# Kernel tuning notes

Measured on AMD Instinct MI355X. Metric: run time of the kernel, lower is better.

The kernel has to match this reference:

```python
import jax, jax.numpy as jnp
import numpy as np

# --- SLAYER params (nmnistNet.yaml) ---
THETA = 10.0
TS = 1.0
TAU_REF = 1.0
SCALE_REF = 2.0
T_SAMPLE = 300
B = 8

def _alpha_kernel(tau, mult, t_sample, ts, eps=0.01):
    vals = []
    t = 0.0
    while t < t_sample:
        v = mult * t / tau * np.exp(1.0 - t / tau)
        if abs(v) < eps and t > tau:
            break
        vals.append(v)
        t += ts
    return np.asarray(vals, np.float32)

# refractory kernel: alpha kernel with mult = -scaleRef*theta (slayer._calculateRefKernel)
REF_KERNEL = _alpha_kernel(TAU_REF, -SCALE_REF * THETA, T_SAMPLE, TS)
NREF = REF_KERNEL.shape[0]  # 11 for these params; REF_KERNEL[0] == 0


def spike(u):
    """slayerCuda.getSpikes: per-neuron sequential threshold recurrence over time.
    u: [..., T] membrane potential. On spike at t, REF_KERNEL is accumulated
    into u[t:t+NREF]; spike amplitude is 1/Ts."""
    uT = jnp.moveaxis(u, -1, 0)  # [T, ...]
    refk = jnp.asarray(REF_KERNEL[1:]).reshape((NREF - 1,) + (1,) * (u.ndim - 1))
    buf0 = jnp.zeros((NREF - 1,) + uT.shape[1:], u.dtype)  # pending refractory

    def step(buf, u_t):
        u_mod = u_t + buf[0]
        ev = (u_mod >= THETA).astype(u.dtype)
        buf = jnp.concatenate([buf[1:], jnp.zeros_like(buf[:1])], axis=0) + ev[None] * refk
        return buf, ev / TS

    _, s = jax.lax.scan(step, buf0, uT)
    return jnp.moveaxis(s, 0, -1)


def conv2d_t(x, w, pad):
    """slayer.conv: Conv3d with kernel (k,k,1) == per-timestep 2D conv.
    x: [B,C,H,W,T], w: [O,I,kh,kw]."""
    b, c, h, wd, t = x.shape
    xb = jnp.moveaxis(x, -1, 1).reshape(b * t, c, h, wd)
    y = jax.lax.conv_general_dilated(xb, w, (1, 1), [(pad, pad), (pad, pad)],
                                     dimension_numbers=('NCHW', 'OIHW', 'NCHW'))
    o, ho, wo = y.shape[1], y.shape[2], y.shape[3]
    return jnp.moveaxis(y.reshape(b, t, o, ho, wo), 1, -1)


def sum_pool2(x):
    """slayer.pool(2): fixed-weight (1.1*theta) 2x2/stride-2 sum over H,W per channel."""
    y = jax.lax.reduce_window(x, 0.0, jax.lax.add, (1, 1, 2, 2, 1), (1, 1, 2, 2, 1), 'VALID')
    return 1.1 * THETA * y


def setup_inputs():
    key = jax.random.key(0)
    k0, k1, k2, k3, k4 = jax.random.split(key, 5)
    spikeInput = (jax.random.uniform(k0, (B, 2, 34, 34, T_SAMPLE)) < 0.1).astype(jnp.float32) / TS
    # conv weights: kaiming-uniform bound * 100 (the __init__ scales conv weights by 100)
    w1 = jax.random.uniform(k1, (16, 2, 5, 5), minval=-14.1, maxval=14.1, dtype=jnp.float32)
    w2 = jax.random.uniform(k2, (32, 16, 3, 3), minval=-8.3, maxval=8.3, dtype=jnp.float32)
    w3 = jax.random.uniform(k3, (64, 32, 3, 3), minval=-5.9, maxval=5.9, dtype=jnp.float32)
    wfc = jax.random.uniform(k4, (10, 64, 8, 8), minval=-0.5, maxval=0.5, dtype=jnp.float32)
    return {"spikeInput": spikeInput, "w1": w1, "w2": w2, "w3": w3, "wfc": wfc}


def reference(spikeInput, w1, w2, w3, wfc):
    s1 = spike(conv2d_t(spikeInput, w1, 1))  # [B,16,32,32,T]
    s2 = spike(sum_pool2(s1))                # [B,16,16,16,T]
    s3 = spike(conv2d_t(s2, w2, 1))          # [B,32,16,16,T]
    s4 = spike(sum_pool2(s3))                # [B,32,8,8,T]
    s5 = spike(conv2d_t(s4, w3, 1))          # [B,64,8,8,T]
    # dense((8,8,64),10): Conv3d(64,10,(8,8,1)) == full-spatial contraction
    u = jnp.einsum('bchwt,ochw->bot', s5, wfc)[:, :, None, None, :]
    return spike(u)                          # [B,10,1,1,T]
```

## Files before the change

### kernel.cpp

```cpp
#include <hip/hip_runtime.h>
#include <hip/hip_bf16.h>
#include <cmath>

#define T_SAMPLE 300
#define NCHUNK 75

typedef __attribute__((ext_vector_type(8))) short short8;
typedef __attribute__((ext_vector_type(4))) float f32x4;

struct RefK { float v[10]; };

__device__ __forceinline__ unsigned char spike_step(float u, float* buf, const RefK& rk) {
    const float um = u + buf[0];
    const bool fire = um >= 10.0f;
    const float ev = fire ? 1.0f : 0.0f;
#pragma unroll
    for (int r = 0; r < 9; ++r) buf[r] = fmaf(ev, rk.v[r], buf[r + 1]);
    buf[9] = ev * rk.v[9];
    return fire ? (unsigned char)1 : (unsigned char)0;
}

__device__ __forceinline__ short8 bytes_to_bf16x8(uint2 w8) {
    union { uint4 u; short8 s8; } cv;
    cv.u.x = (w8.x & 0xFFu) * 0x3F80u | ((((w8.x >> 8) & 0xFFu) * 0x3F80u) << 16);
    cv.u.y = ((w8.x >> 16) & 0xFFu) * 0x3F80u | ((((w8.x >> 24) & 0xFFu) * 0x3F80u) << 16);
    cv.u.z = (w8.y & 0xFFu) * 0x3F80u | ((((w8.y >> 8) & 0xFFu) * 0x3F80u) << 16);
    cv.u.w = ((w8.y >> 16) & 0xFFu) * 0x3F80u | ((((w8.y >> 24) & 0xFFu) * 0x3F80u) << 16);
    return cv.s8;
}

__device__ __forceinline__ unsigned short bf16_split_sel(float w, int s) {
    __hip_bfloat16 hb = __float2bfloat16(w);
    const float hf = __bfloat162float(hb);
    __hip_bfloat16 mb = __float2bfloat16(w - hf);
    const float mf = __bfloat162float(mb);
    __hip_bfloat16 lb = __float2bfloat16(w - hf - mf);
    __hip_bfloat16 sel = (s == 0) ? hb : ((s == 1) ? mb : lb);
    return *(unsigned short*)&sel;
}

__global__ __launch_bounds__(256) void transpose_in_k(
    const float* __restrict__ In, unsigned int* __restrict__ X)
{
    __shared__ unsigned int lds[16 * NCHUNK];
    const int blk = blockIdx.x;
    const int tn = threadIdx.x >> 4;
    const int tq = threadIdx.x & 15;
    const size_t n = (size_t)blk * 16 + tn;
#pragma unroll
    for (int p = 0; p < 5; ++p) {
        const int ch = p * 16 + tq;
        if (ch < NCHUNK) {
            const float4 v = *(const float4*)(In + n * T_SAMPLE + ch * 4);
            unsigned int u = (v.x != 0.f ? 1u : 0u) | (v.y != 0.f ? 0x100u : 0u) |
                             (v.z != 0.f ? 0x10000u : 0u) | (v.w != 0.f ? 0x1000000u : 0u);
            lds[tn * NCHUNK + ch] = u;
        }
    }
    __syncthreads();
    for (int idx = threadIdx.x; idx < 16 * NCHUNK; idx += 256) {
        const int ch = idx >> 4, t2 = idx & 15;
        X[(size_t)ch * 18496 + blk * 16 + t2] = lds[t2 * NCHUNK + ch];
    }
}

__global__ __launch_bounds__(256) void prep_w1_k(
    const float* __restrict__ w1, unsigned short* __restrict__ Wr1)
{
    const int g = blockIdx.x * 256 + threadIdx.x;
    const int j = g & 7;
    const int lane = (g >> 3) & 63;
    const int ks = (g >> 9) & 3;
    const int s = g >> 11;
    const int q = lane >> 4;
    const int oc = lane & 15;
    const int kg = ks * 32 + q * 8 + j;
    const int slot = kg >> 2, c = kg & 1;
    const int dy = slot / 6, dx = slot % 6;
    const float w = (dy < 5 && dx < 5) ? w1[((oc * 2 + c) * 5 + dy) * 5 + dx] * 0.5f : 0.f;
    Wr1[g] = bf16_split_sel(w, s);
}

__global__ __launch_bounds__(256) void prep_w3_k(
    const float* __restrict__ w3, unsigned short* __restrict__ Wr)
{
    const int g = blockIdx.x * 256 + threadIdx.x;
    const int j = g & 7;
    const int lane = (g >> 3) & 63;
    const int mt = (g >> 9) & 3;
    const int rest = g >> 11;
    const int ks = rest % 9;
    const int s = rest / 9;
    const int oc = mt * 16 + (lane & 15);
    const int ic = (lane >> 4) * 8 + j;
    Wr[g] = bf16_split_sel(w3[(oc * 32 + ic) * 9 + ks], s);
}

__global__ __launch_bounds__(256) void prep_w2_k(
    const float* __restrict__ w2, unsigned short* __restrict__ Wr2)
{
    const int g = blockIdx.x * 256 + threadIdx.x;
    const int j = g & 7;
    const int lane = (g >> 3) & 63;
    const int mt = (g >> 9) & 1;
    const int rest = g >> 10;
    const int kp = rest % 5;
    const int s = rest / 5;
    const int q = lane >> 4;
    const int oc = mt * 16 + (lane & 15);
    const int tap = kp * 2 + (q >> 1);
    const int ic = (q & 1) * 8 + j;
    const float w = (tap <= 8) ? w2[(oc * 16 + ic) * 9 + tap] : 0.f;
    Wr2[g] = bf16_split_sel(w, s);
}

__device__ __forceinline__ void c1_mfma_chunk(
    const unsigned int* __restrict__ tb, const int* offA, const int* offB,
    const short8* Af, f32x4* acc)
{
    unsigned int vA[4][4], vB[4][4];
#pragma unroll
    for (int ks = 0; ks < 4; ++ks)
#pragma unroll
        for (int t = 0; t < 4; ++t) {
            vA[ks][t] = tb[t * 72 + offA[ks]];
            vB[ks][t] = tb[t * 72 + offB[ks]];
        }

#pragma unroll
    for (int t = 0; t < 4; ++t) acc[t] = (f32x4){0.f, 0.f, 0.f, 0.f};
#pragma unroll
    for (int ks = 0; ks < 4; ++ks)
#pragma unroll
        for (int t = 0; t < 4; ++t) {
            union { uint4 u; short8 s8; } cv;
            cv.u.x = vA[ks][t]; cv.u.y = vA[ks][t];
            cv.u.z = vB[ks][t]; cv.u.w = vB[ks][t];
#pragma unroll
            for (int s = 0; s < 3; ++s)
                acc[t] = __builtin_amdgcn_mfma_f32_16x16x32_bf16(
                    Af[s * 4 + ks], cv.s8, acc[t], 0, 0, 0);
        }
}

__global__ __launch_bounds__(512, 4) void conv1pc_k(
    const unsigned int* __restrict__ X, const unsigned short* __restrict__ Wr1,
    uchar4* __restrict__ S1, RefK rk)
{
    __shared__ unsigned int tab[2][5 * 288];
    __shared__ __align__(16) float4 Ulds[2][5 * 256];
    const int pg = blockIdx.x;
    const int b = blockIdx.y;
    const int ty = pg >> 2, tx = pg & 3;
    const int tid = threadIdx.x;
    const int wv = tid >> 6, lane = tid & 63;
    const bool isConv = (wv >= 4);
    const int q = lane >> 4, n = lane & 15;
    const int py0 = n >> 3, px0 = n & 7;

    short8 Af[12];
    int offA[4], offB[4];
    int lidx[2], gof[2];
    unsigned int w0[2], w1[2];
    if (isConv) {
#pragma unroll
        for (int s = 0; s < 3; ++s)
#pragma unroll
            for (int ks = 0; ks < 4; ++ks)
                Af[s * 4 + ks] = *(const short8*)(Wr1 + (((s * 4 + ks) * 64 + lane) * 8));
#pragma unroll
        for (int ks = 0; ks < 4; ++ks) {
            const int sA = ks * 8 + q * 2, sB = sA + 1;
            const int dyA = sA / 6, dxA = sA - dyA * 6;
            const int dyB = sB / 6, dxB = sB - dyB * 6;
            offA[ks] = min(py0 + dyA, 5) * 12 + min(px0 + dxA, 11);
            offB[ks] = min(py0 + dyB, 5) * 12 + min(px0 + dxB, 11);
        }
        const int tid2 = tid - 256;
#pragma unroll
        for (int i = 0; i < 2; ++i) {
            const int e = i * 256 + tid2;
            if (e < 360) {
                const int chl = e / 72, site = e - chl * 72;
                const int r = site / 12, cc = site - r * 12;
                const int gy = ty * 2 - 1 + r, gx = tx * 8 - 1 + cc;
                lidx[i] = chl * 288 + site;
                gof[i] = (((unsigned)gy < 34u) && ((unsigned)gx < 34u))
                       ? (chl * 18496 + (b * 2) * 1156 + gy * 34 + gx) : -1;
            } else { lidx[i] = -1; gof[i] = -1; }
        }
#pragma unroll
        for (int i = 0; i < 2; ++i) {
            if (gof[i] >= 0) { w0[i] = X[gof[i]]; w1[i] = X[gof[i] + 1156]; }
            else { w0[i] = 0u; w1[i] = 0u; }
        }
#pragma unroll
        for (int i = 0; i < 2; ++i) {
            if (lidx[i] >= 0) {
#pragma unroll
                for (int t = 0; t < 4; ++t)
                    tab[0][lidx[i] + t * 72] =
                        ((w0[i] >> (8 * t)) & 0xFFu) * 0x3F80u
                        | ((((w1[i] >> (8 * t)) & 0xFFu) * 0x3F80u) << 16);
            }
        }
    }

    float buf[10];
#pragma unroll
    for (int r = 0; r < 10; ++r) buf[r] = 0.f;
    const int s_oc = (tid & 255) >> 4, s_n = tid & 15;
    const int nb0 = (b * 16 + s_oc) * 1024 + (ty * 2 + (s_n >> 3)) * 32 + tx * 8 + (s_n & 7);

    __syncthreads();

    for (int w = 0; w < 15; ++w) {
        const int cb = w & 1;
        if (isConv) {
            if (w < 14) {
                const unsigned int* Xs = X + (size_t)(w + 1) * (5 * 18496);
#pragma unroll
                for (int i = 0; i < 2; ++i) {
                    if (gof[i] >= 0) { w0[i] = Xs[gof[i]]; w1[i] = Xs[gof[i] + 1156]; }
                }
            }
            for (int k = wv - 4; k < 5; k += 4) {
                f32x4 acc[4];
                c1_mfma_chunk(&tab[cb][k * 288], offA, offB, Af, acc);
#pragma unroll
                for (int rr = 0; rr < 4; ++rr)
                    Ulds[cb][k * 256 + (q * 4 + rr) * 16 + n] =
                        make_float4(acc[0][rr], acc[1][rr], acc[2][rr], acc[3][rr]);
            }
            if (w < 14) {
#pragma unroll
                for (int i = 0; i < 2; ++i) {
                    if (lidx[i] >= 0) {
#pragma unroll
                        for (int t = 0; t < 4; ++t)
                            tab[cb ^ 1][lidx[i] + t * 72] =
                                ((w0[i] >> (8 * t)) & 0xFFu) * 0x3F80u
                                | ((((w1[i] >> (8 * t)) & 0xFFu) * 0x3F80u) << 16);
                    }
                }
            }
        } else if (w > 0) {
            const int pb = (w - 1) & 1;
            for (int k = 0; k < 5; ++k) {
                const float4 u = Ulds[pb][k * 256 + tid];
                uchar4 o;
                o.x = spike_step(u.x, buf, rk);
                o.y = spike_step(u.y, buf, rk);
                o.z = spike_step(u.z, buf, rk);
                o.w = spike_step(u.w, buf, rk);
                S1[(size_t)((w - 1) * 5 + k) * 131072 + nb0] = o;
            }
        }
        __syncthreads();
    }
    if (!isConv) {
        for (int k = 0; k < 5; ++k) {
            const float4 u = Ulds[0][k * 256 + tid];
            uchar4 o;
            o.x = spike_step(u.x, buf, rk);
            o.y = spike_step(u.y, buf, rk);
            o.z = spike_step(u.z, buf, rk);
            o.w = spike_step(u.w, buf, rk);
            S1[(size_t)(70 + k) * 131072 + nb0] = o;
        }
    }
}

__global__ __launch_bounds__(256) void conv2_mfma_k(
    const unsigned int* __restrict__ s2u, const unsigned short* __restrict__ Wr2,
    float4* __restrict__ U, int b0, int nbl)
{
    __shared__ __align__(16) unsigned char pad[4 * 18 * 18 * 16];
    const int tc = blockIdx.x;
    const int bl = blockIdx.z;
    const int b = b0 + bl;
    const int tid = threadIdx.x;
    const int wv = tid >> 6, lane = tid & 63;
    const int q = lane >> 4, n = lane & 15;
    const int PLANE_U = nbl * 8192;

    unsigned int* lp = (unsigned int*)pad;
    for (int i = tid; i < 5184; i += 256) lp[i] = 0u;
    __syncthreads();
    const unsigned int* sb = s2u + (size_t)tc * 32768 + b * 4096;
    for (int e = tid; e < 4096; e += 256) {
        const unsigned int v = sb[e];
        const int c = e >> 8, pix = e & 255;
        const int base = (((pix >> 4) + 1) * 18 + ((pix & 15) + 1)) * 16 + c;
        pad[base]         = (unsigned char)(v & 0xFFu);
        pad[5184 + base]  = (unsigned char)((v >> 8) & 0xFFu);
        pad[10368 + base] = (unsigned char)((v >> 16) & 0xFFu);
        pad[15552 + base] = (unsigned char)(v >> 24);
    }
    __syncthreads();

    for (int i = 0; i < 4; ++i) {
        const int r = wv * 4 + i;
        f32x4 acc[2][4];
#pragma unroll
        for (int mt = 0; mt < 2; ++mt)
#pragma unroll
            for (int t = 0; t < 4; ++t) acc[mt][t] = (f32x4){0.f, 0.f, 0.f, 0.f};

        for (int kp = 0; kp < 5; ++kp) {
            short8 Af[6];
#pragma unroll
            for (int s = 0; s < 3; ++s)
#pragma unroll
                for (int mt = 0; mt < 2; ++mt)
                    Af[s * 2 + mt] = *(const short8*)(Wr2 + ((((s * 5 + kp) * 2 + mt) * 64 + lane) * 8));
            int tap = kp * 2 + (q >> 1);
            if (tap > 8) tap = 8;
            const int dy = tap / 3, dx = tap % 3;
#pragma unroll
            for (int t = 0; t < 4; ++t) {
                const int off = ((t * 18 + r + dy) * 18 + (n + dx)) * 16 + (q & 1) * 8;
                const short8 Bf = bytes_to_bf16x8(*(const uint2*)(pad + off));
#pragma unroll
                for (int s = 0; s < 3; ++s)
#pragma unroll
                    for (int mt = 0; mt < 2; ++mt)
                        acc[mt][t] = __builtin_amdgcn_mfma_f32_16x16x32_bf16(
                            Af[s * 2 + mt], Bf, acc[mt][t], 0, 0, 0);
            }
        }

        const size_t ub = (size_t)tc * PLANE_U;
#pragma unroll
        for (int mt = 0; mt < 2; ++mt)
#pragma unroll
            for (int rr = 0; rr < 4; ++rr) {
                const int oc = mt * 16 + q * 4 + rr;
                const int nb = (bl * 32 + oc) * 256 + r * 16 + n;
                U[ub + nb] = make_float4(acc[mt][0][rr], acc[mt][1][rr], acc[mt][2][rr], acc[mt][3][rr]);
            }
    }
}

__global__ __launch_bounds__(256) void conv3_mfma_k(
    const unsigned int* __restrict__ s4u, const unsigned short* __restrict__ Wr,
    float4* __restrict__ U)
{
    __shared__ __align__(16) unsigned char pad[12800];
    const int tc = blockIdx.x;
    const int bl = blockIdx.z;
    const int tid = threadIdx.x;
    const int wv = tid >> 6, lane = tid & 63;
    const int q = lane >> 4, n = lane & 15;

    unsigned int* lp = (unsigned int*)pad;
    for (int i = tid; i < 3200; i += 256) lp[i] = 0u;
    __syncthreads();
    const unsigned int* sb = s4u + (size_t)tc * 16384 + bl * 2048;
    for (int e = tid; e < 2048; e += 256) {
        const unsigned int v = sb[e];
        const int c = e >> 6, pix = e & 63;
        const int base = (((pix >> 3) + 1) * 10 + ((pix & 7) + 1)) * 32 + c;
        pad[base]        = (unsigned char)(v & 0xFFu);
        pad[3200 + base] = (unsigned char)((v >> 8) & 0xFFu);
        pad[6400 + base] = (unsigned char)((v >> 16) & 0xFFu);
        pad[9600 + base] = (unsigned char)(v >> 24);
    }
    __syncthreads();

    const int pixel = wv * 16 + n;
    const int py0 = pixel >> 3, px0 = pixel & 7;

    f32x4 acc[4][4];
#pragma unroll
    for (int mt = 0; mt < 4; ++mt)
#pragma unroll
        for (int t = 0; t < 4; ++t) acc[mt][t] = (f32x4){0.f, 0.f, 0.f, 0.f};

    for (int ks = 0; ks < 9; ++ks) {
        const int dy = ks / 3, dx = ks % 3;
        short8 Af[12];
#pragma unroll
        for (int s = 0; s < 3; ++s)
#pragma unroll
            for (int mt = 0; mt < 4; ++mt)
                Af[s * 4 + mt] = *(const short8*)(Wr + ((((s * 9 + ks) * 4 + mt) * 64 + lane) * 8));
#pragma unroll
        for (int t = 0; t < 4; ++t) {
            const int off = ((t * 10 + py0 + dy) * 10 + (px0 + dx)) * 32 + q * 8;
            const short8 Bf = bytes_to_bf16x8(*(const uint2*)(pad + off));
#pragma unroll
            for (int s = 0; s < 3; ++s)
#pragma unroll
                for (int mt = 0; mt < 4; ++mt)
                    acc[mt][t] = __builtin_amdgcn_mfma_f32_16x16x32_bf16(
                        Af[s * 4 + mt], Bf, acc[mt][t], 0, 0, 0);
        }
    }

    const size_t ub = (size_t)tc * 32768 + (size_t)bl * 4096;
#pragma unroll
    for (int mt = 0; mt < 4; ++mt)
#pragma unroll
        for (int r = 0; r < 4; ++r) {
            const int oc = mt * 16 + q * 4 + r;
            const int nb = oc * 64 + wv * 16 + n;
            U[ub + nb] = make_float4(acc[mt][0][r], acc[mt][1][r], acc[mt][2][r], acc[mt][3][r]);
        }
}

__device__ __forceinline__ void spike_body(
    const float4* __restrict__ U, uchar4* __restrict__ S,
    int nneur, int sstride, int soff, const RefK& rk)
{
    const int n = blockIdx.x * 64 + threadIdx.x;
    const float4* up = U + n;
    uchar4* sp = S + soff + n;
    float buf[10];
#pragma unroll
    for (int r = 0; r < 10; ++r) buf[r] = 0.f;

    float4 ring[8];
#pragma unroll
    for (int r = 0; r < 8; ++r) ring[r] = up[(size_t)r * nneur];

#pragma unroll 8
    for (int ch = 0; ch < 72; ++ch) {
        const float4 cur = ring[ch & 7];
        const int pf = (ch + 8 < NCHUNK) ? ch + 8 : NCHUNK - 1;
        ring[ch & 7] = up[(size_t)pf * nneur];
        uchar4 o;
        o.x = spike_step(cur.x, buf, rk);
        o.y = spike_step(cur.y, buf, rk);
        o.z = spike_step(cur.z, buf, rk);
        o.w = spike_step(cur.w, buf, rk);
        sp[(size_t)ch * sstride] = o;
    }
#pragma unroll
    for (int ch = 72; ch < NCHUNK; ++ch) {
        const float4 cur = ring[ch & 7];
        uchar4 o;
        o.x = spike_step(cur.x, buf, rk);
        o.y = spike_step(cur.y, buf, rk);
        o.z = spike_step(cur.z, buf, rk);
        o.w = spike_step(cur.w, buf, rk);
        sp[(size_t)ch * sstride] = o;
    }
}

__global__ __launch_bounds__(64) void spike2_k(
    const float4* U, uchar4* S, int nneur, int sstride, int soff, RefK rk)
{ spike_body(U, S, nneur, sstride, soff, rk); }

__global__ __launch_bounds__(64) void spike3_k(
    const float4* U, uchar4* S, int nneur, int sstride, int soff, RefK rk)
{ spike_body(U, S, nneur, sstride, soff, rk); }

__device__ __forceinline__ int bsum4(uint2 r0, uint2 r1, int k) {
    return (int)((r0.x >> (8 * k)) & 0xffu) + (int)((r0.y >> (8 * k)) & 0xffu)
         + (int)((r1.x >> (8 * k)) & 0xffu) + (int)((r1.y >> (8 * k)) & 0xffu);
}

template <int C, int H, int W>
__device__ __forceinline__ void pool_body(
    const uchar4* __restrict__ Sin, uchar4* __restrict__ Sout, const RefK& rk)
{
    constexpr int H2 = H / 2, W2 = W / 2;
    constexpr int SIN = 8 * C * H * W;
    constexpr int SOUT = 8 * C * H2 * W2;
    const int n = blockIdx.x * 64 + threadIdx.x;
    const int x = n % W2;
    const int y = (n / W2) % H2;
    const int c = (n / (W2 * H2)) % C;
    const int b = n / (W2 * H2 * C);
    const int base = (((b * C + c) * H + 2 * y) * W + 2 * x);
    uchar4* q = Sout + n;

    float buf[10];
#pragma unroll
    for (int r = 0; r < 10; ++r) buf[r] = 0.f;

    uint2 r0[8], r1[8];
#pragma unroll
    for (int r = 0; r < 8; ++r) {
        r0[r] = *(const uint2*)(Sin + (size_t)r * SIN + base);
        r1[r] = *(const uint2*)(Sin + (size_t)r * SIN + base + W);
    }

#pragma unroll 8
    for (int ch = 0; ch < 72; ++ch) {
        const uint2 a0 = r0[ch & 7], a1 = r1[ch & 7];
        const int pf = (ch + 8 < NCHUNK) ? ch + 8 : NCHUNK - 1;
        r0[ch & 7] = *(const uint2*)(Sin + (size_t)pf * SIN + base);
        r1[ch & 7] = *(const uint2*)(Sin + (size_t)pf * SIN + base + W);
        uchar4 o;
        o.x = spike_step(11.0f * (float)bsum4(a0, a1, 0), buf, rk);
        o.y = spike_step(11.0f * (float)bsum4(a0, a1, 1), buf, rk);
        o.z = spike_step(11.0f * (float)bsum4(a0, a1, 2), buf, rk);
        o.w = spike_step(11.0f * (float)bsum4(a0, a1, 3), buf, rk);
        q[(size_t)ch * SOUT] = o;
    }
#pragma unroll
    for (int ch = 72; ch < NCHUNK; ++ch) {
        const uint2 a0 = r0[ch & 7], a1 = r1[ch & 7];
        uchar4 o;
        o.x = spike_step(11.0f * (float)bsum4(a0, a1, 0), buf, rk);
        o.y = spike_step(11.0f * (float)bsum4(a0, a1, 1), buf, rk);
        o.z = spike_step(11.0f * (float)bsum4(a0, a1, 2), buf, rk);
        o.w = spike_step(11.0f * (float)bsum4(a0, a1, 3), buf, rk);
        q[(size_t)ch * SOUT] = o;
    }
}

__global__ __launch_bounds__(64) void pool2_k(
    const uchar4* Sin, uchar4* Sout, RefK rk) { pool_body<16, 32, 32>(Sin, Sout, rk); }
__global__ __launch_bounds__(64) void pool4_k(
    const uchar4* Sin, uchar4* Sout, RefK rk) { pool_body<32, 16, 16>(Sin, Sout, rk); }

__global__ __launch_bounds__(64) void dense_k(
    const uchar4* __restrict__ S5, const float* __restrict__ WFC,
    float4* __restrict__ U6)
{
    const int tc = blockIdx.x, o = blockIdx.y, b = blockIdx.z;
    const int lane = threadIdx.x;
    float a0 = 0.f, a1 = 0.f, a2 = 0.f, a3 = 0.f;
    const uchar4* sb = S5 + (size_t)tc * 32768 + b * 4096;
    const float* wb = WFC + o * 4096;
    for (int i = 0; i < 64; ++i) {
        const int site = i * 64 + lane;
        const uchar4 s = sb[site];
        const float w = wb[site];
        a0 = fmaf(w, (float)s.x, a0);
        a1 = fmaf(w, (float)s.y, a1);
        a2 = fmaf(w, (float)s.z, a2);
        a3 = fmaf(w, (float)s.w, a3);
    }
#pragma unroll
    for (int m = 1; m < 64; m <<= 1) {
        a0 += __shfl_xor(a0, m, 64);
        a1 += __shfl_xor(a1, m, 64);
        a2 += __shfl_xor(a2, m, 64);
        a3 += __shfl_xor(a3, m, 64);
    }
    if (lane == 0)
        U6[(size_t)tc * 80 + b * 10 + o] = make_float4(a0, a1, a2, a3);
}

__global__ __launch_bounds__(128) void spike6_k(
    const float4* __restrict__ U6, float* __restrict__ Out, RefK rk)
{
    const int n = threadIdx.x;
    if (n >= 80) return;
    const float4* up = U6 + n;
    float* op = Out + (size_t)n * T_SAMPLE;
    float buf[10];
#pragma unroll
    for (int r = 0; r < 10; ++r) buf[r] = 0.f;

    float4 ring[8];
#pragma unroll
    for (int r = 0; r < 8; ++r) ring[r] = up[(size_t)r * 80];

#pragma unroll 8
    for (int ch = 0; ch < 72; ++ch) {
        const float4 cur = ring[ch & 7];
        const int pf = (ch + 8 < NCHUNK) ? ch + 8 : NCHUNK - 1;
        ring[ch & 7] = up[(size_t)pf * 80];
        float4 o;
        o.x = (float)spike_step(cur.x, buf, rk);
        o.y = (float)spike_step(cur.y, buf, rk);
        o.z = (float)spike_step(cur.z, buf, rk);
        o.w = (float)spike_step(cur.w, buf, rk);
        *(float4*)(op + ch * 4) = o;
    }
#pragma unroll
    for (int ch = 72; ch < NCHUNK; ++ch) {
        const float4 cur = ring[ch & 7];
        float4 o;
        o.x = (float)spike_step(cur.x, buf, rk);
        o.y = (float)spike_step(cur.y, buf, rk);
        o.z = (float)spike_step(cur.z, buf, rk);
        o.w = (float)spike_step(cur.w, buf, rk);
        *(float4*)(op + ch * 4) = o;
    }
}

extern "C" void kernel_launch(void* const* d_in, const int* in_sizes, int n_in,
                              void* d_out, int out_size, void* d_ws, size_t ws_size,
                              hipStream_t stream)
{
    const float* spikeIn = (const float*)d_in[0];
    const float* w1 = (const float*)d_in[1];
    const float* w2 = (const float*)d_in[2];
    const float* w3 = (const float*)d_in[3];
    const float* wfc = (const float*)d_in[4];
    float* out = (float*)d_out;

    RefK rk;
    for (int t = 1; t <= 10; ++t)
        rk.v[t - 1] = (float)(-20.0 * (double)t * std::exp(1.0 - (double)t));

    const size_t A_BYTES = 39321600;
    const size_t B_BYTES = 9830400;
    const size_t U6_BYTES = 96000;
    const size_t U_BIG = 78643200, U_SMALL = 39321600;
    const size_t TAIL = A_BYTES + B_BYTES + U6_BYTES;
    const bool big = ws_size >= U_BIG + TAIL;
    const size_t U_BYTES = big ? U_BIG : U_SMALL;

    char* ws = (char*)d_ws;
    float4* U = (float4*)ws;
    uchar4* A = (uchar4*)(ws + U_BYTES);
    uchar4* Bb = (uchar4*)(ws + U_BYTES + A_BYTES);
    float4* U6 = (float4*)(ws + U_BYTES + A_BYTES + B_BYTES);
    unsigned short* Wr = (unsigned short*)(ws + U_BYTES + 20971520);
    unsigned short* Wr2 = (unsigned short*)(ws + U_BYTES + 20971520 + 131072);
    unsigned short* Wr1 = (unsigned short*)(ws + U_BYTES + A_BYTES + 5570560);

    uchar4* X = Bb;
    uchar4* s1 = A;
    uchar4* s2 = Bb;
    uchar4* s3 = A;
    uchar4* s4 = Bb;
    uchar4* s5 = A;

    transpose_in_k<<<18496 / 16, 256, 0, stream>>>(spikeIn, (unsigned int*)X);
    prep_w1_k<<<24, 256, 0, stream>>>(w1, Wr1);

    {
        dim3 g1(64, 8);
        conv1pc_k<<<g1, 512, 0, stream>>>((const unsigned int*)X, Wr1, s1, rk);
    }
    pool2_k<<<32768 / 64, 64, 0, stream>>>(s1, s2, rk);
    prep_w2_k<<<60, 256, 0, stream>>>(w2, Wr2);
    prep_w3_k<<<216, 256, 0, stream>>>(w3, Wr);
    const int nbl2 = big ? 8 : 4;
    for (int b0 = 0; b0 < 8; b0 += nbl2) {
        dim3 g2(NCHUNK, 1, nbl2);
        conv2_mfma_k<<<g2, 256, 0, stream>>>((const unsigned int*)s2, Wr2, U, b0, nbl2);
        const int nn = nbl2 * 8192;
        spike2_k<<<nn / 64, 64, 0, stream>>>(U, s3, nn, 65536, b0 * 8192, rk);
    }
    pool4_k<<<16384 / 64, 64, 0, stream>>>(s3, s4, rk);
    {
        dim3 g3(NCHUNK, 1, 8);
        conv3_mfma_k<<<g3, 256, 0, stream>>>((const unsigned int*)s4, Wr, U);
        spike3_k<<<32768 / 64, 64, 0, stream>>>(U, s5, 32768, 32768, 0, rk);
    }
    {
        dim3 g6(NCHUNK, 10, 8);
        dense_k<<<g6, 64, 0, stream>>>(s5, wfc, U6);
    }
    spike6_k<<<1, 128, 0, stream>>>(U6, out, rk);
}
```

Measured before the change: 249.9 us.

## Fuse 2x2 sum-pool spiking into conv1 and conv2 spike epilogues

Folds the pool2 and pool4 stages into the preceding spike kernels. Each thread computes its conv spike, gathers the 2x2 neighbourhood's spike bytes via wave shuffles, and a subset of lanes runs the pooled neuron's refractory recurrence and writes the pooled spikes directly. This removes two kernel launches and the global write and reread of the full-resolution s1 and s3 spike tensors. In exchange, only a quarter of the lanes do the pooled spike work, which adds serial work and divergence inside the spike phases.

```diff
diff --git a/kernel.cpp b/kernel.cpp
--- a/kernel.cpp
+++ b/kernel.cpp
@@ -18,6 +18,11 @@
     for (int r = 0; r < 9; ++r) buf[r] = fmaf(ev, rk.v[r], buf[r + 1]);
     buf[9] = ev * rk.v[9];
     return fire ? (unsigned char)1 : (unsigned char)0;
+}
+
+__device__ __forceinline__ int psum4(int g0, int g1, int g2, int g3, int sh) {
+    return ((g0 >> sh) & 0xff) + ((g1 >> sh) & 0xff)
+         + ((g2 >> sh) & 0xff) + ((g3 >> sh) & 0xff);
 }
 
 __device__ __forceinline__ short8 bytes_to_bf16x8(uint2 w8) {
@@ -145,7 +150,7 @@
 
 __global__ __launch_bounds__(512, 4) void conv1pc_k(
     const unsigned int* __restrict__ X, const unsigned short* __restrict__ Wr1,
-    uchar4* __restrict__ S1, RefK rk)
+    uchar4* __restrict__ S2, RefK rk)
 {
     __shared__ unsigned int tab[2][5 * 288];
     __shared__ __align__(16) float4 Ulds[2][5 * 256];
@@ -206,11 +211,33 @@
         }
     }
 
-    float buf[10];
-#pragma unroll
-    for (int r = 0; r < 10; ++r) buf[r] = 0.f;
-    const int s_oc = (tid & 255) >> 4, s_n = tid & 15;
-    const int nb0 = (b * 16 + s_oc) * 1024 + (ty * 2 + (s_n >> 3)) * 32 + tx * 8 + (s_n & 7);
+    float buf[10], buf2[10];
+#pragma unroll
+    for (int r = 0; r < 10; ++r) { buf[r] = 0.f; buf2[r] = 0.f; }
+    const int s_oc = (tid & 255) >> 4;
+    const int lb = lane & 48;
+    const int xq = lane & 3;
+    const size_t s2base = ((size_t)(b * 16 + s_oc) * 16 + ty) * 16 + (tx * 4 + (lane & 15));
+
+    auto spike_pool = [&](int ch, const float4& u) {
+        union { uchar4 c; int i; } o;
+        o.c.x = spike_step(u.x, buf, rk);
+        o.c.y = spike_step(u.y, buf, rk);
+        o.c.z = spike_step(u.z, buf, rk);
+        o.c.w = spike_step(u.w, buf, rk);
+        const int g0 = __shfl(o.i, lb + 2 * xq, 64);
+        const int g1 = __shfl(o.i, lb + 2 * xq + 1, 64);
+        const int g2 = __shfl(o.i, lb + 8 + 2 * xq, 64);
+        const int g3 = __shfl(o.i, lb + 9 + 2 * xq, 64);
+        if ((lane & 15) < 4) {
+            uchar4 po;
+            po.x = spike_step(11.0f * (float)psum4(g0, g1, g2, g3, 0), buf2, rk);
+            po.y = spike_step(11.0f * (float)psum4(g0, g1, g2, g3, 8), buf2, rk);
+            po.z = spike_step(11.0f * (float)psum4(g0, g1, g2, g3, 16), buf2, rk);
+            po.w = spike_step(11.0f * (float)psum4(g0, g1, g2, g3, 24), buf2, rk);
+            S2[(size_t)ch * 32768 + s2base] = po;
+        }
+    };
 
     __syncthreads();
 
@@ -246,28 +273,14 @@
             }
         } else if (w > 0) {
             const int pb = (w - 1) & 1;
-            for (int k = 0; k < 5; ++k) {
-                const float4 u = Ulds[pb][k * 256 + tid];
-                uchar4 o;
-                o.x = spike_step(u.x, buf, rk);
-                o.y = spike_step(u.y, buf, rk);
-                o.z = spike_step(u.z, buf, rk);
-                o.w = spike_step(u.w, buf, rk);
-                S1[(size_t)((w - 1) * 5 + k) * 131072 + nb0] = o;
-            }
+            for (int k = 0; k < 5; ++k)
+                spike_pool((w - 1) * 5 + k, Ulds[pb][k * 256 + tid]);
         }
         __syncthreads();
     }
     if (!isConv) {
-        for (int k = 0; k < 5; ++k) {
-            const float4 u = Ulds[0][k * 256 + tid];
-            uchar4 o;
-            o.x = spike_step(u.x, buf, rk);
-            o.y = spike_step(u.y, buf, rk);
-            o.z = spike_step(u.z, buf, rk);
-            o.w = spike_step(u.w, buf, rk);
-            S1[(size_t)(70 + k) * 131072 + nb0] = o;
-        }
+        for (int k = 0; k < 5; ++k)
+            spike_pool(70 + k, Ulds[0][k * 256 + tid]);
     }
 }
 
@@ -409,9 +422,64 @@
         }
 }
 
-__device__ __forceinline__ void spike_body(
+__global__ __launch_bounds__(64) void spike2p_k(
+    const float4* __restrict__ U, uchar4* __restrict__ S4,
+    int nneur, int b0, RefK rk)
+{
+    const int lane = threadIdx.x;
+    const int n = blockIdx.x * 64 + lane;
+    const float4* up = U + n;
+    float buf[10], buf2[10];
+#pragma unroll
+    for (int r = 0; r < 10; ++r) { buf[r] = 0.f; buf2[r] = 0.f; }
+
+    const int bl = n >> 13, oc = (n >> 8) & 31, y = (n >> 4) & 15;
+    const int b = b0 + bl;
+    const int y0 = y & ~3;
+    const int p = lane & 15, ppy = p >> 3, ppx = p & 7;
+    const int sB = 32 * ppy + 2 * ppx;
+    const size_t s4base = (size_t)(b * 32 + oc) * 64 + ((y0 >> 1) + ppy) * 8 + ppx;
+
+    auto step_pool = [&](int ch, const float4& cur) {
+        union { uchar4 c; int i; } o;
+        o.c.x = spike_step(cur.x, buf, rk);
+        o.c.y = spike_step(cur.y, buf, rk);
+        o.c.z = spike_step(cur.z, buf, rk);
+        o.c.w = spike_step(cur.w, buf, rk);
+        const int g0 = __shfl(o.i, sB, 64);
+        const int g1 = __shfl(o.i, sB + 1, 64);
+        const int g2 = __shfl(o.i, sB + 16, 64);
+        const int g3 = __shfl(o.i, sB + 17, 64);
+        if (lane < 16) {
+            uchar4 po;
+            po.x = spike_step(11.0f * (float)psum4(g0, g1, g2, g3, 0), buf2, rk);
+            po.y = spike_step(11.0f * (float)psum4(g0, g1, g2, g3, 8), buf2, rk);
+            po.z = spike_step(11.0f * (float)psum4(g0, g1, g2, g3, 16), buf2, rk);
+            po.w = spike_step(11.0f * (float)psum4(g0, g1, g2, g3, 24), buf2, rk);
+            S4[(size_t)ch * 16384 + s4base] = po;
+        }
+    };
+
+    float4 ring[8];
+#pragma unroll
+    for (int r = 0; r < 8; ++r) ring[r] = up[(size_t)r * nneur];
+
+#pragma unroll 8
+    for (int ch = 0; ch < 72; ++ch) {
+        const float4 cur = ring[ch & 7];
+        const int pf = (ch + 8 < NCHUNK) ? ch + 8 : NCHUNK - 1;
+        ring[ch & 7] = up[(size_t)pf * nneur];
+        step_pool(ch, cur);
+    }
+#pragma unroll
+    for (int ch = 72; ch < NCHUNK; ++ch) {
+        step_pool(ch, ring[ch & 7]);
+    }
+}
+
+__global__ __launch_bounds__(64) void spike3_k(
     const float4* __restrict__ U, uchar4* __restrict__ S,
-    int nneur, int sstride, int soff, const RefK& rk)
+    int nneur, int sstride, int soff, RefK rk)
 {
     const int n = blockIdx.x * 64 + threadIdx.x;
     const float4* up = U + n;
@@ -447,75 +515,6 @@
         sp[(size_t)ch * sstride] = o;
     }
 }
-
-__global__ __launch_bounds__(64) void spike2_k(
-    const float4* U, uchar4* S, int nneur, int sstride, int soff, RefK rk)
-{ spike_body(U, S, nneur, sstride, soff, rk); }
-
-__global__ __launch_bounds__(64) void spike3_k(
-    const float4* U, uchar4* S, int nneur, int sstride, int soff, RefK rk)
-{ spike_body(U, S, nneur, sstride, soff, rk); }
-
-__device__ __forceinline__ int bsum4(uint2 r0, uint2 r1, int k) {
-    return (int)((r0.x >> (8 * k)) & 0xffu) + (int)((r0.y >> (8 * k)) & 0xffu)
-         + (int)((r1.x >> (8 * k)) & 0xffu) + (int)((r1.y >> (8 * k)) & 0xffu);
-}
-
-template <int C, int H, int W>
-__device__ __forceinline__ void pool_body(
-    const uchar4* __restrict__ Sin, uchar4* __restrict__ Sout, const RefK& rk)
-{
-    constexpr int H2 = H / 2, W2 = W / 2;
-    constexpr int SIN = 8 * C * H * W;
-    constexpr int SOUT = 8 * C * H2 * W2;
-    const int n = blockIdx.x * 64 + threadIdx.x;
-    const int x = n % W2;
-    const int y = (n / W2) % H2;
-    const int c = (n / (W2 * H2)) % C;
-    const int b = n / (W2 * H2 * C);
-    const int base = (((b * C + c) * H + 2 * y) * W + 2 * x);
-    uchar4* q = Sout + n;
-
-    float buf[10];
-#pragma unroll
-    for (int r = 0; r < 10; ++r) buf[r] = 0.f;
-
-    uint2 r0[8], r1[8];
-#pragma unroll
-    for (int r = 0; r < 8; ++r) {
-        r0[r] = *(const uint2*)(Sin + (size_t)r * SIN + base);
-        r1[r] = *(const uint2*)(Sin + (size_t)r * SIN + base + W);
-    }
-
-#pragma unroll 8
-    for (int ch = 0; ch < 72; ++ch) {
-        const uint2 a0 = r0[ch & 7], a1 = r1[ch & 7];
-        const int pf = (ch + 8 < NCHUNK) ? ch + 8 : NCHUNK - 1;
-        r0[ch & 7] = *(const uint2*)(Sin + (size_t)pf * SIN + base);
-        r1[ch & 7] = *(const uint2*)(Sin + (size_t)pf * SIN + base + W);
-        uchar4 o;
-        o.x = spike_step(11.0f * (float)bsum4(a0, a1, 0), buf, rk);
-        o.y = spike_step(11.0f * (float)bsum4(a0, a1, 1), buf, rk);
-        o.z = spike_step(11.0f * (float)bsum4(a0, a1, 2), buf, rk);
-        o.w = spike_step(11.0f * (float)bsum4(a0, a1, 3), buf, rk);
-        q[(size_t)ch * SOUT] = o;
-    }
-#pragma unroll
-    for (int ch = 72; ch < NCHUNK; ++ch) {
-        const uint2 a0 = r0[ch & 7], a1 = r1[ch & 7];
-        uchar4 o;
-        o.x = spike_step(11.0f * (float)bsum4(a0, a1, 0), buf, rk);
-        o.y = spike_step(11.0f * (float)bsum4(a0, a1, 1), buf, rk);
-        o.z = spike_step(11.0f * (float)bsum4(a0, a1, 2), buf, rk);
-        o.w = spike_step(11.0f * (float)bsum4(a0, a1, 3), buf, rk);
-        q[(size_t)ch * SOUT] = o;
-    }
-}
-
-__global__ __launch_bounds__(64) void pool2_k(
-    const uchar4* Sin, uchar4* Sout, RefK rk) { pool_body<16, 32, 32>(Sin, Sout, rk); }
-__global__ __launch_bounds__(64) void pool4_k(
-    const uchar4* Sin, uchar4* Sout, RefK rk) { pool_body<32, 16, 16>(Sin, Sout, rk); }
 
 __global__ __launch_bounds__(64) void dense_k(
     const uchar4* __restrict__ S5, const float* __restrict__ WFC,
@@ -610,28 +609,25 @@
 
     char* ws = (char*)d_ws;
     float4* U = (float4*)ws;
-    uchar4* A = (uchar4*)(ws + U_BYTES);
-    uchar4* Bb = (uchar4*)(ws + U_BYTES + A_BYTES);
+    char* Ab = ws + U_BYTES;
+    char* Bb = ws + U_BYTES + A_BYTES;
     float4* U6 = (float4*)(ws + U_BYTES + A_BYTES + B_BYTES);
-    unsigned short* Wr = (unsigned short*)(ws + U_BYTES + 20971520);
-    unsigned short* Wr2 = (unsigned short*)(ws + U_BYTES + 20971520 + 131072);
-    unsigned short* Wr1 = (unsigned short*)(ws + U_BYTES + A_BYTES + 5570560);
-
-    uchar4* X = Bb;
-    uchar4* s1 = A;
-    uchar4* s2 = Bb;
-    uchar4* s3 = A;
-    uchar4* s4 = Bb;
-    uchar4* s5 = A;
-
-    transpose_in_k<<<18496 / 16, 256, 0, stream>>>(spikeIn, (unsigned int*)X);
+    unsigned short* Wr = (unsigned short*)(Ab + 20971520);
+    unsigned short* Wr2 = (unsigned short*)(Ab + 20971520 + 131072);
+    unsigned short* Wr1 = (unsigned short*)(Bb + 5570560);
+
+    unsigned int* X = (unsigned int*)Bb;
+    uchar4* s2 = (uchar4*)Ab;
+    uchar4* s4 = (uchar4*)Bb;
+    uchar4* s5 = (uchar4*)Ab;
+
+    transpose_in_k<<<18496 / 16, 256, 0, stream>>>(spikeIn, X);
     prep_w1_k<<<24, 256, 0, stream>>>(w1, Wr1);
 
     {
         dim3 g1(64, 8);
-        conv1pc_k<<<g1, 512, 0, stream>>>((const unsigned int*)X, Wr1, s1, rk);
-    }
-    pool2_k<<<32768 / 64, 64, 0, stream>>>(s1, s2, rk);
+        conv1pc_k<<<g1, 512, 0, stream>>>(X, Wr1, s2, rk);
+    }
     prep_w2_k<<<60, 256, 0, stream>>>(w2, Wr2);
     prep_w3_k<<<216, 256, 0, stream>>>(w3, Wr);
     const int nbl2 = big ? 8 : 4;
@@ -639,9 +635,8 @@
         dim3 g2(NCHUNK, 1, nbl2);
         conv2_mfma_k<<<g2, 256, 0, stream>>>((const unsigned int*)s2, Wr2, U, b0, nbl2);
         const int nn = nbl2 * 8192;
-        spike2_k<<<nn / 64, 64, 0, stream>>>(U, s3, nn, 65536, b0 * 8192, rk);
-    }
-    pool4_k<<<16384 / 64, 64, 0, stream>>>(s3, s4, rk);
+        spike2p_k<<<nn / 64, 64, 0, stream>>>(U, s4, nn, b0, rk);
+    }
     {
         dim3 g3(NCHUNK, 1, 8);
         conv3_mfma_k<<<g3, 256, 0, stream>>>((const unsigned int*)s4, Wr, U);
```

Result: slower. 266.7 us (+6.7%).
